# Optimization experiments

Measured on AMD Instinct MI355X. Metric: run time of the kernel, lower is better.

The kernel has to match this reference:

```python
import jax, jax.numpy as jnp
import numpy as np

B, S, H, NH, HD, P, MAXP = 2, 2048, 2048, 16, 128, 2048, 4096
EPS = 1e-06


def setup_inputs() -> dict:
    key = jax.random.key(0)
    ks = jax.random.split(key, 8)
    sc = lambda fan: 1.0 / np.sqrt(fan)
    hidden_states = jax.random.normal(ks[0], (B, S, H), jnp.float32)
    # rotary table: freqs[p] = p * inv_freq, duplicated (non-interleaved) -> [MAXP,1,1,HD]
    inv_freq = 1.0 / (500000.0 ** (np.arange(0, HD, 2, dtype=np.float32) / HD))
    ang = np.outer(np.arange(MAXP, dtype=np.float32), inv_freq)  # [MAXP, HD/2]
    freqs = jnp.asarray(np.concatenate([ang, ang], axis=-1).reshape(MAXP, 1, 1, HD), jnp.float32)
    positions = jnp.tile(jnp.arange(S, dtype=jnp.int32), B)  # [T] = [B*S]
    Wqk = jax.random.normal(ks[1], (2 * P, H), jnp.float32) * sc(H)
    Wv = jax.random.normal(ks[2], (P, H), jnp.float32) * sc(H)
    Wo = jax.random.normal(ks[3], (H, P), jnp.float32) * sc(P)
    conv1_w = jax.random.normal(ks[4], (H // 2, H, 2, 1), jnp.float32) * sc(2 * H)
    conv1_b = jax.random.normal(ks[5], (H // 2,), jnp.float32) * 0.01
    conv2_w = jax.random.normal(ks[6], (H, H // 2, 2, 1), jnp.float32) * sc(H)
    conv2_b = jax.random.normal(ks[7], (H,), jnp.float32) * 0.01
    ln_w = jnp.ones((H,), jnp.float32)
    lf1_cache = jnp.zeros((B, H, 1, 1), jnp.float32)
    lf2_cache = jnp.zeros((B, H // 2, 1, 1), jnp.float32)
    return dict(hidden_states=hidden_states, freqs=freqs, positions=positions,
                Wqk=Wqk, Wv=Wv, Wo=Wo, conv1_w=conv1_w, conv1_b=conv1_b,
                conv2_w=conv2_w, conv2_b=conv2_b, ln_w=ln_w,
                lf1_cache=lf1_cache, lf2_cache=lf2_cache)


def _rmsnorm(x, w, eps=EPS):
    return x * w * jax.lax.rsqrt(jnp.mean(x * x, axis=-1, keepdims=True) + eps)


def _rotate_half(x):
    x1, x2 = jnp.split(x, 2, axis=-1)
    return jnp.concatenate([-x2, x1], axis=-1)


def _forward(hidden_states, freqs, positions, Wqk, Wv, Wo,
             conv1_w, conv1_b, conv2_w, conv2_b, ln_w, lf1_cache, lf2_cache):
    # v projection on raw hidden states
    v = jnp.einsum('bsh,ph->bsp', hidden_states, Wv)  # [B,S,P]

    # --- LocalizedFiltering (causal (2,1) convs with 1-step caches) ---
    x = hidden_states                                     # [B,S,H]
    xc = jnp.concatenate([lf1_cache[:, :, 0, 0][:, None, :], x], axis=1)  # [B,S+1,H]
    w1a, w1b = conv1_w[:, :, 0, 0], conv1_w[:, :, 1, 0]   # [H/2,H]
    y1 = (jnp.einsum('bsh,oh->bso', xc[:, :-1], w1a)
          + jnp.einsum('bsh,oh->bso', xc[:, 1:], w1b) + conv1_b)  # [B,S,H/2]
    y1c = jnp.concatenate([lf2_cache[:, :, 0, 0][:, None, :], y1], axis=1)  # [B,S+1,H/2]
    w2a, w2b = conv2_w[:, :, 0, 0], conv2_w[:, :, 1, 0]   # [H,H/2]
    y2 = (jnp.einsum('bso,ho->bsh', y1c[:, :-1], w2a)
          + jnp.einsum('bso,ho->bsh', y1c[:, 1:], w2b) + conv2_b)  # [B,S,H]
    lf_out = _rmsnorm(y2 + x, ln_w)                       # [B,S,H]
    lf1_new = xc[:, -1][:, :, None, None]                 # [B,H,1,1]
    lf2_new = y1c[:, -1][:, :, None, None]                # [B,H/2,1,1]

    # --- QK projection + RoPE ---
    qk = jnp.einsum('bsh,ph->bsp', lf_out, Wqk).reshape(B, S, NH, 2 * HD)
    q, k = jnp.split(qk, 2, axis=-1)                      # [B,S,NH,HD] each
    f = freqs[positions].reshape(B, S, 1, HD)             # per-token angles
    cos_, sin_ = jnp.cos(f), jnp.sin(f)
    q = q * cos_ + _rotate_half(q) * sin_
    k = k * cos_ + _rotate_half(k) * sin_

    # --- causal SDPA ---
    scale = HD ** -0.5
    vh = v.reshape(B, S, NH, HD)
    scores = jnp.einsum('bqhd,bkhd->bhqk', q, k) * scale  # [B,NH,S,S]
    mask = jnp.tril(jnp.ones((S, S), bool))
    scores = jnp.where(mask, scores, jnp.float32(-1e30))
    probs = jax.nn.softmax(scores, axis=-1)
    attn = jnp.einsum('bhqk,bkhd->bqhd', probs, vh).reshape(B * S, P)

    output = attn @ Wo.T                                  # [T,H]
    return output, lf1_new, lf2_new


def reference(hidden_states, freqs, positions, Wqk, Wv, Wo,
              conv1_w, conv1_b, conv2_w, conv2_b, ln_w, lf1_cache, lf2_cache):
    return _forward(hidden_states, freqs, positions, Wqk, Wv, Wo,
                    conv1_w, conv1_b, conv2_w, conv2_b, ln_w, lf1_cache, lf2_cache)
```

## Files before the change

kernel.cpp:

```cpp
#include <hip/hip_runtime.h>
#include <hip/hip_bf16.h>
#include <stdint.h>

#define Bb 2
#define Ss 2048
#define Hh 2048
#define NHh 16
#define HDd 128
#define Pp 2048
#define Mm 4096

typedef __bf16 bf16x8 __attribute__((ext_vector_type(8)));
typedef float f32x4 __attribute__((ext_vector_type(4)));
typedef float f32x16 __attribute__((ext_vector_type(16)));
typedef __hip_bfloat16 bf16_t;

static __device__ __forceinline__ bf16_t f2b(float f) { return __float2bfloat16(f); }
static __device__ __forceinline__ float b2f(bf16_t b) { return __bfloat162float(b); }


__global__ void k_f2b(const float* __restrict__ src, bf16_t* __restrict__ dst, int n) {
  int stride = gridDim.x * blockDim.x;
  for (int i = blockIdx.x * blockDim.x + threadIdx.x; i < n; i += stride)
    dst[i] = f2b(src[i]);
}

__global__ void k_pack_conv1(const float* __restrict__ w, bf16_t* __restrict__ dst) {
  int stride = gridDim.x * blockDim.x;
  for (int i = blockIdx.x * blockDim.x + threadIdx.x; i < 1024 * 4096; i += stride) {
    int o = i >> 12, hp = i & 4095;
    int t = hp >> 11, h = hp & 2047;
    dst[i] = f2b(w[((size_t)o * 2048 + h) * 2 + t]);
  }
}

__global__ void k_pack_conv2(const float* __restrict__ w, bf16_t* __restrict__ dst) {
  int stride = gridDim.x * blockDim.x;
  for (int i = blockIdx.x * blockDim.x + threadIdx.x; i < 2048 * 2048; i += stride) {
    int o = i >> 11, cp = i & 2047;
    int t = cp >> 10, c = cp & 1023;
    dst[i] = f2b(w[((size_t)o * 1024 + c) * 2 + t]);
  }
}

__global__ void k_pack_x(const float* __restrict__ x, const float* __restrict__ lf1,
                         bf16_t* __restrict__ xcat) {
  int stride = gridDim.x * blockDim.x;
  for (int i = blockIdx.x * blockDim.x + threadIdx.x; i < Mm * Hh; i += stride) {
    int m = i >> 11, h = i & 2047;
    int b = m >> 11, s = m & 2047;
    float xv = x[i];
    xcat[(size_t)m * 4096 + 2048 + h] = f2b(xv);
    float xs = (s == 0) ? lf1[b * 2048 + h] : x[i - 2048];
    xcat[(size_t)m * 4096 + h] = f2b(xs);
  }
}

__global__ void k_pack_y1cat(const float* __restrict__ y1, const float* __restrict__ lf2,
                             bf16_t* __restrict__ y1cat) {
  int stride = gridDim.x * blockDim.x;
  for (int i = blockIdx.x * blockDim.x + threadIdx.x; i < Mm * 1024; i += stride) {
    int m = i >> 10, c = i & 1023;
    int b = m >> 11, s = m & 2047;
    y1cat[(size_t)m * 2048 + 1024 + c] = f2b(y1[i]);
    float ys = (s == 0) ? lf2[b * 1024 + c] : y1[i - 1024];
    y1cat[(size_t)m * 2048 + c] = f2b(ys);
  }
}

__global__ __launch_bounds__(256) void k_rmsnorm(const float* __restrict__ y2,
                                                 const float* __restrict__ x,
                                                 const float* __restrict__ w,
                                                 bf16_t* __restrict__ out) {
  int m = blockIdx.x;
  const float* yr = y2 + (size_t)m * 2048;
  const float* xr = x + (size_t)m * 2048;
  int tid = threadIdx.x;
  float t[8];
  float ss = 0.0f;
#pragma unroll
  for (int j = 0; j < 8; ++j) {
    int idx = tid + j * 256;
    float v = yr[idx] + xr[idx];
    t[j] = v;
    ss += v * v;
  }
#pragma unroll
  for (int o = 32; o >= 1; o >>= 1) ss += __shfl_xor(ss, o, 64);
  __shared__ float red[4];
  if ((tid & 63) == 0) red[tid >> 6] = ss;
  __syncthreads();
  float tot = red[0] + red[1] + red[2] + red[3];
  float rs = rsqrtf(tot * (1.0f / 2048.0f) + 1e-6f);
#pragma unroll
  for (int j = 0; j < 8; ++j) {
    int idx = tid + j * 256;
    out[(size_t)m * 2048 + idx] = f2b(t[j] * w[idx] * rs);
  }
}

__global__ __launch_bounds__(256) void k_rope(const bf16_t* __restrict__ qk,
                                              const float* __restrict__ freqs,
                                              const int* __restrict__ positions,
                                              bf16_t* __restrict__ qa, bf16_t* __restrict__ ka) {
  int m = blockIdx.x;
  int b = m >> 11, s = m & 2047;
  int pos = positions[m];
  const float* fr = freqs + (size_t)pos * HDd;
  const bf16_t* row = qk + (size_t)m * 4096;
  const float scale = 0.08838834764831845f;
#pragma unroll
  for (int it = 0; it < 8; ++it) {
    int p = it * 256 + threadIdx.x;
    int isk = p >> 10;
    int pp = p & 1023;
    int h = pp >> 6, d = pp & 63;
    float f = fr[d];
    float c = cosf(f), sn = sinf(f);
    float v0 = b2f(row[h * 256 + isk * 128 + d]);
    float v1 = b2f(row[h * 256 + isk * 128 + 64 + d]);
    float o0 = v0 * c - v1 * sn;
    float o1 = v1 * c + v0 * sn;
    float sc = isk ? 1.0f : scale;
    bf16_t* dst = (isk ? ka : qa) + ((size_t)(b * NHh + h) * Ss + s) * HDd;
    dst[d] = f2b(o0 * sc);
    dst[64 + d] = f2b(o1 * sc);
  }
}

__global__ __launch_bounds__(256) void k_vt(const bf16_t* __restrict__ v, bf16_t* __restrict__ vt) {
  int bh = blockIdx.x;
  int s0 = blockIdx.y * 64;
  int b = bh >> 4, h = bh & 15;
  __shared__ bf16_t tile[128][65];
#pragma unroll
  for (int it = 0; it < 32; ++it) {
    int idx = it * 256 + threadIdx.x;
    int sl = idx >> 7, d = idx & 127;
    tile[d][sl] = v[((size_t)(b * 2048 + s0 + sl)) * 2048 + h * 128 + d];
  }
  __syncthreads();
#pragma unroll
  for (int it = 0; it < 32; ++it) {
    int idx = it * 256 + threadIdx.x;
    int d = idx >> 6, sl = idx & 63;
    vt[((size_t)bh * 128 + d) * 2048 + s0 + sl] = tile[d][sl];
  }
}

__global__ void k_tails(const float* __restrict__ x, const float* __restrict__ y1,
                        float* __restrict__ out) {
  int i = blockIdx.x * 256 + threadIdx.x;
  if (i >= 4096 + 2048) return;
  const size_t off = (size_t)Mm * Hh;
  if (i < 4096) {
    int b = i >> 11, h = i & 2047;
    out[off + i] = x[((size_t)b * 2048 + 2047) * 2048 + h];
  } else {
    int j = i - 4096;
    int b = j >> 10, c = j & 1023;
    out[off + 4096 + j] = y1[((size_t)b * 2048 + 2047) * 1024 + c];
  }
}

template <int BF16_OUT, int HAS_BIAS>
__global__ __launch_bounds__(256) void gemm_bt_kernel(const bf16_t* __restrict__ A,
                                                      const bf16_t* __restrict__ Bw,
                                                      void* __restrict__ Cout,
                                                      const float* __restrict__ bias,
                                                      int M, int N, int K, int lda) {
  __shared__ bf16_t lA[128 * 64];
  __shared__ bf16_t lB[128 * 64];
  const int tid = threadIdx.x;
  const int lane = tid & 63;
  const int row0 = blockIdx.x * 128;
  const int col0 = blockIdx.y * 128;
  const int wr = ((tid >> 6) >> 1) * 64;
  const int wc = ((tid >> 6) & 1) * 64;
  const int lr = lane & 15;
  const int lg = lane >> 4;

  f32x4 acc[4][4];
#pragma unroll
  for (int i = 0; i < 4; ++i)
#pragma unroll
    for (int j = 0; j < 4; ++j) acc[i][j] = f32x4{0.f, 0.f, 0.f, 0.f};

  for (int k0 = 0; k0 < K; k0 += 64) {
    __syncthreads();
#pragma unroll
    for (int is = 0; is < 4; ++is) {
      const int e = is * 2048 + tid * 8;
      const int r = e >> 6, c = e & 63;
      __builtin_amdgcn_global_load_lds(
          (const __attribute__((address_space(1))) void*)(A + (size_t)(row0 + r) * lda + (k0 + c)),
          (__attribute__((address_space(3))) void*)(&lA[e]), 16, 0, 0);
      __builtin_amdgcn_global_load_lds(
          (const __attribute__((address_space(1))) void*)(Bw + (size_t)(col0 + r) * K + (k0 + c)),
          (__attribute__((address_space(3))) void*)(&lB[e]), 16, 0, 0);
    }
    __syncthreads();
#pragma unroll
    for (int ks = 0; ks < 2; ++ks) {
      bf16x8 af[4], bfg[4];
#pragma unroll
      for (int mi = 0; mi < 4; ++mi)
        af[mi] = *reinterpret_cast<const bf16x8*>(&lA[(wr + mi * 16 + lr) * 64 + ks * 32 + lg * 8]);
#pragma unroll
      for (int ni = 0; ni < 4; ++ni)
        bfg[ni] = *reinterpret_cast<const bf16x8*>(&lB[(wc + ni * 16 + lr) * 64 + ks * 32 + lg * 8]);
#pragma unroll
      for (int mi = 0; mi < 4; ++mi)
#pragma unroll
        for (int ni = 0; ni < 4; ++ni)
          acc[mi][ni] = __builtin_amdgcn_mfma_f32_16x16x32_bf16(af[mi], bfg[ni], acc[mi][ni], 0, 0, 0);
    }
  }
#pragma unroll
  for (int mi = 0; mi < 4; ++mi) {
#pragma unroll
    for (int ni = 0; ni < 4; ++ni) {
      const int cc = col0 + wc + ni * 16 + lr;
      float bv = HAS_BIAS ? bias[cc] : 0.0f;
#pragma unroll
      for (int r = 0; r < 4; ++r) {
        const int rr = row0 + wr + mi * 16 + lg * 4 + r;
        float v = acc[mi][ni][r] + bv;
        if (BF16_OUT)
          ((bf16_t*)Cout)[(size_t)rr * N + cc] = f2b(v);
        else
          ((float*)Cout)[(size_t)rr * N + cc] = v;
      }
    }
  }
}

__global__ __launch_bounds__(256) void k_attn2(const bf16_t* __restrict__ qa,
                                               const bf16_t* __restrict__ ka,
                                               const bf16_t* __restrict__ vt,
                                               bf16_t* __restrict__ attn_out) {
  __shared__ bf16_t kbuf[64 * 128];
  __shared__ bf16_t vbuf[128 * 64];
  __shared__ bf16_t pbuf[4][32 * 64];

  const int tid = threadIdx.x;
  const int wave = tid >> 6, lane = tid & 63;
  const int l31 = lane & 31, hi = lane >> 5;
  const int bh = blockIdx.x;
  const int q0b = blockIdx.y * 128;
  const int q0w = q0b + wave * 32;
  const int b = bh >> 4, h = bh & 15;

  const bf16_t* Q = qa + (size_t)bh * Ss * HDd;
  const bf16_t* K = ka + (size_t)bh * Ss * HDd;
  const bf16_t* V = vt + (size_t)bh * HDd * Ss;
  char* pw = (char*)&pbuf[wave][0];

  bf16x8 qf[8];
#pragma unroll
  for (int dc = 0; dc < 8; ++dc)
    qf[dc] = *reinterpret_cast<const bf16x8*>(&Q[(size_t)(q0w + l31) * HDd + dc * 16 + hi * 8]);

  f32x16 o[4];
#pragma unroll
  for (int db = 0; db < 4; ++db)
#pragma unroll
    for (int i = 0; i < 16; ++i) o[db][i] = 0.f;
  float mrun = -3e38f, lrun = 0.f;
  const int qrow = q0w + l31;

  const int nkt = q0b / 64 + 2;
  for (int kt = 0; kt < nkt; ++kt) {
    const int k0 = kt * 64;
    __syncthreads();
#pragma unroll
    for (int i = 0; i < 4; ++i) {
      const int kr = tid >> 2, ku = (tid & 3) + 4 * i;
      bf16x8 tk = *reinterpret_cast<const bf16x8*>(&K[(size_t)(k0 + kr) * HDd + ku * 8]);
      *reinterpret_cast<bf16x8*>((char*)kbuf + kr * 256 + ((ku * 16) ^ ((kr & 7) << 4))) = tk;
      const int vr = tid >> 1, vu = (tid & 1) * 4 + i;
      bf16x8 tv = *reinterpret_cast<const bf16x8*>(&V[(size_t)vr * Ss + k0 + vu * 8]);
      *reinterpret_cast<bf16x8*>((char*)vbuf + vr * 128 + ((vu * 16) ^ ((vr & 7) << 4))) = tv;
    }
    __syncthreads();
    if (k0 > q0w + 31) continue;

    f32x16 s0, s1;
#pragma unroll
    for (int i = 0; i < 16; ++i) { s0[i] = 0.f; s1[i] = 0.f; }
#pragma unroll
    for (int dc = 0; dc < 8; ++dc) {
      const int off = (dc * 32 + hi * 16) ^ ((l31 & 7) << 4);
      bf16x8 kf0 = *reinterpret_cast<const bf16x8*>((const char*)kbuf + l31 * 256 + off);
      bf16x8 kf1 = *reinterpret_cast<const bf16x8*>((const char*)kbuf + (32 + l31) * 256 + off);
      s0 = __builtin_amdgcn_mfma_f32_32x32x16_bf16(kf0, qf[dc], s0, 0, 0, 0);
      s1 = __builtin_amdgcn_mfma_f32_32x32x16_bf16(kf1, qf[dc], s1, 0, 0, 0);
    }
    if (k0 + 63 > q0w) {
#pragma unroll
      for (int reg = 0; reg < 16; ++reg) {
        const int key = k0 + (reg & 3) + 8 * (reg >> 2) + 4 * hi;
        if (key > qrow) s0[reg] = -1e30f;
        if (key + 32 > qrow) s1[reg] = -1e30f;
      }
    }
    float pm = fmaxf(s0[0], s1[0]);
#pragma unroll
    for (int reg = 1; reg < 16; ++reg) pm = fmaxf(pm, fmaxf(s0[reg], s1[reg]));
    pm = fmaxf(pm, __shfl_xor(pm, 32, 64));
    if (!__all(pm - mrun <= 8.0f)) {
      const float mnew = fmaxf(mrun, pm);
      const float alpha = __expf(mrun - mnew);
      lrun *= alpha;
#pragma unroll
      for (int reg = 0; reg < 16; ++reg) {
        const int r = (reg & 3) + 8 * (reg >> 2) + 4 * hi;
        const float ar = __shfl(alpha, r, 64);
        o[0][reg] *= ar; o[1][reg] *= ar; o[2][reg] *= ar; o[3][reg] *= ar;
      }
      mrun = mnew;
    }
    float psum = 0.f;
#pragma unroll
    for (int reg = 0; reg < 16; ++reg) {
      s0[reg] = __expf(s0[reg] - mrun); psum += s0[reg];
      s1[reg] = __expf(s1[reg] - mrun); psum += s1[reg];
    }
    psum += __shfl_xor(psum, 32, 64);
    lrun += psum;
#pragma unroll
    for (int g = 0; g < 4; ++g) {
      uint32_t w0, w1, w2, w3;
      asm("v_cvt_pk_bf16_f32 %0, %1, %2" : "=v"(w0) : "v"(s0[4 * g]), "v"(s0[4 * g + 1]));
      asm("v_cvt_pk_bf16_f32 %0, %1, %2" : "=v"(w1) : "v"(s0[4 * g + 2]), "v"(s0[4 * g + 3]));
      asm("v_cvt_pk_bf16_f32 %0, %1, %2" : "=v"(w2) : "v"(s1[4 * g]), "v"(s1[4 * g + 1]));
      asm("v_cvt_pk_bf16_f32 %0, %1, %2" : "=v"(w3) : "v"(s1[4 * g + 2]), "v"(s1[4 * g + 3]));
      const int key0 = 8 * g + 4 * hi;
      const int sw = (l31 & 7) << 4;
      *reinterpret_cast<uint2*>(pw + l31 * 128 + ((key0 * 2) ^ sw)) = uint2{w0, w1};
      *reinterpret_cast<uint2*>(pw + l31 * 128 + (((key0 + 32) * 2) ^ sw)) = uint2{w2, w3};
    }
#pragma unroll
    for (int kc = 0; kc < 4; ++kc) {
      bf16x8 pa = *reinterpret_cast<const bf16x8*>(
          pw + l31 * 128 + ((kc * 32 + hi * 16) ^ ((l31 & 7) << 4)));
#pragma unroll
      for (int db = 0; db < 4; ++db) {
        const int d = db * 32 + l31;
        bf16x8 vf = *reinterpret_cast<const bf16x8*>(
            (const char*)vbuf + d * 128 + ((kc * 32 + hi * 16) ^ ((d & 7) << 4)));
        o[db] = __builtin_amdgcn_mfma_f32_32x32x16_bf16(pa, vf, o[db], 0, 0, 0);
      }
    }
  }
  const float linv = 1.0f / lrun;
#pragma unroll
  for (int reg = 0; reg < 16; ++reg) {
    const int r = (reg & 3) + 8 * (reg >> 2) + 4 * hi;
    const float li = __shfl(linv, r, 64);
    const int qr = q0w + r;
#pragma unroll
    for (int db = 0; db < 4; ++db) {
      attn_out[(size_t)(b * 2048 + qr) * 2048 + h * 128 + db * 32 + l31] = f2b(o[db][reg] * li);
    }
  }
}

extern "C" void kernel_launch(void* const* d_in, const int* in_sizes, int n_in,
                              void* d_out, int out_size, void* d_ws, size_t ws_size,
                              hipStream_t stream) {
  const float* x     = (const float*)d_in[0];
  const float* freqs = (const float*)d_in[1];
  const int*   pos   = (const int*)d_in[2];
  const float* Wqk   = (const float*)d_in[3];
  const float* Wv    = (const float*)d_in[4];
  const float* Wo    = (const float*)d_in[5];
  const float* c1w   = (const float*)d_in[6];
  const float* c1b   = (const float*)d_in[7];
  const float* c2w   = (const float*)d_in[8];
  const float* c2b   = (const float*)d_in[9];
  const float* lnw   = (const float*)d_in[10];
  const float* lf1   = (const float*)d_in[11];
  const float* lf2   = (const float*)d_in[12];
  float* out = (float*)d_out;

  char* ws = (char*)d_ws;
  const size_t MB = 1024 * 1024;
  bf16_t* wv_bf  = (bf16_t*)(ws + 0 * MB);
  bf16_t* wqk_bf = (bf16_t*)(ws + 8 * MB);
  bf16_t* wo_bf  = (bf16_t*)(ws + 24 * MB);
  bf16_t* w1cat  = (bf16_t*)(ws + 32 * MB);
  bf16_t* w2cat  = (bf16_t*)(ws + 40 * MB);
  bf16_t* xcat   = (bf16_t*)(ws + 48 * MB);
  bf16_t* v_bf   = (bf16_t*)(ws + 80 * MB);
  float*  y1_f   = (float*)(ws + 96 * MB);
  bf16_t* y1cat  = (bf16_t*)(ws + 112 * MB);
  float*  y2_f   = (float*)(ws + 48 * MB);
  bf16_t* lfo_bf = (bf16_t*)(ws + 96 * MB);
  bf16_t* qk_bf  = (bf16_t*)(ws + 48 * MB);
  bf16_t* vt_att = (bf16_t*)(ws + 112 * MB);
  bf16_t* q_att  = (bf16_t*)(ws + 80 * MB);
  bf16_t* k_att  = (bf16_t*)(ws + 8 * MB);
  bf16_t* attn_b = (bf16_t*)(ws + 48 * MB);

  k_f2b<<<2048, 256, 0, stream>>>(Wv, wv_bf, 2048 * 2048);
  k_f2b<<<2048, 256, 0, stream>>>(Wqk, wqk_bf, 4096 * 2048);
  k_f2b<<<2048, 256, 0, stream>>>(Wo, wo_bf, 2048 * 2048);
  k_pack_conv1<<<2048, 256, 0, stream>>>(c1w, w1cat);
  k_pack_conv2<<<2048, 256, 0, stream>>>(c2w, w2cat);
  k_pack_x<<<2048, 256, 0, stream>>>(x, lf1, xcat);

  gemm_bt_kernel<1, 0><<<dim3(Mm / 128, 2048 / 128), 256, 0, stream>>>(
      xcat + 2048, wv_bf, v_bf, nullptr, Mm, 2048, 2048, 4096);
  gemm_bt_kernel<0, 1><<<dim3(Mm / 128, 1024 / 128), 256, 0, stream>>>(
      xcat, w1cat, y1_f, c1b, Mm, 1024, 4096, 4096);
  k_tails<<<24, 256, 0, stream>>>(x, y1_f, out);
  k_pack_y1cat<<<2048, 256, 0, stream>>>(y1_f, lf2, y1cat);
  gemm_bt_kernel<0, 1><<<dim3(Mm / 128, 2048 / 128), 256, 0, stream>>>(
      y1cat, w2cat, y2_f, c2b, Mm, 2048, 2048, 2048);
  k_rmsnorm<<<Mm, 256, 0, stream>>>(y2_f, x, lnw, lfo_bf);
  gemm_bt_kernel<1, 0><<<dim3(Mm / 128, 4096 / 128), 256, 0, stream>>>(
      lfo_bf, wqk_bf, qk_bf, nullptr, Mm, 4096, 2048, 2048);
  k_vt<<<dim3(Bb * NHh, Ss / 64), 256, 0, stream>>>(v_bf, vt_att);
  k_rope<<<Mm, 256, 0, stream>>>(qk_bf, freqs, pos, q_att, k_att);
  k_attn2<<<dim3(Bb * NHh, Ss / 128), 256, 0, stream>>>(q_att, k_att, vt_att, attn_b);
  gemm_bt_kernel<0, 0><<<dim3(Mm / 128, 2048 / 128), 256, 0, stream>>>(
      attn_b, wo_bf, out, nullptr, Mm, 2048, 2048, 2048);
}
```

Baseline: 680.9 us.

## Fuse RoPE, V transpose and y1cat packing into GEMM epilogues; pipeline attention loads

Adds epilogue variants to the GEMM template so the QK GEMM applies RoPE and writes head-major q/k directly, the V GEMM writes the transposed V layout, and the conv1 GEMM writes the shifted bf16 concat buffer itself. This removes the separate rope, transpose and pack kernels along with their intermediate round-trips through global memory. The attention kernel now issues the next K/V tile's global loads early into registers, raises wave priority around the MFMA blocks, and launches the longest causal query blocks first for load balance. It also reshuffles workspace offsets. The new epilogues add LDS staging and a sync, and y1 now flows through bf16 instead of fp32, which affects precision.

New measurement: 642.7 us. -5.6%, faster.

```diff
diff --git a/kernel.cpp b/kernel.cpp
--- a/kernel.cpp
+++ b/kernel.cpp
@@ -56,16 +56,11 @@
   }
 }
 
-__global__ void k_pack_y1cat(const float* __restrict__ y1, const float* __restrict__ lf2,
-                             bf16_t* __restrict__ y1cat) {
-  int stride = gridDim.x * blockDim.x;
-  for (int i = blockIdx.x * blockDim.x + threadIdx.x; i < Mm * 1024; i += stride) {
-    int m = i >> 10, c = i & 1023;
-    int b = m >> 11, s = m & 2047;
-    y1cat[(size_t)m * 2048 + 1024 + c] = f2b(y1[i]);
-    float ys = (s == 0) ? lf2[b * 1024 + c] : y1[i - 1024];
-    y1cat[(size_t)m * 2048 + c] = f2b(ys);
-  }
+__global__ void k_lf2fill(const float* __restrict__ lf2, bf16_t* __restrict__ y1cat) {
+  int i = blockIdx.x * 256 + threadIdx.x;
+  if (i >= 2048) return;
+  int b = i >> 10, c = i & 1023;
+  y1cat[(size_t)(b * 2048) * 2048 + c] = f2b(lf2[b * 1024 + c]);
 }
 
 __global__ __launch_bounds__(256) void k_rmsnorm(const float* __restrict__ y2,
@@ -99,56 +94,7 @@
   }
 }
 
-__global__ __launch_bounds__(256) void k_rope(const bf16_t* __restrict__ qk,
-                                              const float* __restrict__ freqs,
-                                              const int* __restrict__ positions,
-                                              bf16_t* __restrict__ qa, bf16_t* __restrict__ ka) {
-  int m = blockIdx.x;
-  int b = m >> 11, s = m & 2047;
-  int pos = positions[m];
-  const float* fr = freqs + (size_t)pos * HDd;
-  const bf16_t* row = qk + (size_t)m * 4096;
-  const float scale = 0.08838834764831845f;
-#pragma unroll
-  for (int it = 0; it < 8; ++it) {
-    int p = it * 256 + threadIdx.x;
-    int isk = p >> 10;
-    int pp = p & 1023;
-    int h = pp >> 6, d = pp & 63;
-    float f = fr[d];
-    float c = cosf(f), sn = sinf(f);
-    float v0 = b2f(row[h * 256 + isk * 128 + d]);
-    float v1 = b2f(row[h * 256 + isk * 128 + 64 + d]);
-    float o0 = v0 * c - v1 * sn;
-    float o1 = v1 * c + v0 * sn;
-    float sc = isk ? 1.0f : scale;
-    bf16_t* dst = (isk ? ka : qa) + ((size_t)(b * NHh + h) * Ss + s) * HDd;
-    dst[d] = f2b(o0 * sc);
-    dst[64 + d] = f2b(o1 * sc);
-  }
-}
-
-__global__ __launch_bounds__(256) void k_vt(const bf16_t* __restrict__ v, bf16_t* __restrict__ vt) {
-  int bh = blockIdx.x;
-  int s0 = blockIdx.y * 64;
-  int b = bh >> 4, h = bh & 15;
-  __shared__ bf16_t tile[128][65];
-#pragma unroll
-  for (int it = 0; it < 32; ++it) {
-    int idx = it * 256 + threadIdx.x;
-    int sl = idx >> 7, d = idx & 127;
-    tile[d][sl] = v[((size_t)(b * 2048 + s0 + sl)) * 2048 + h * 128 + d];
-  }
-  __syncthreads();
-#pragma unroll
-  for (int it = 0; it < 32; ++it) {
-    int idx = it * 256 + threadIdx.x;
-    int d = idx >> 6, sl = idx & 63;
-    vt[((size_t)bh * 128 + d) * 2048 + s0 + sl] = tile[d][sl];
-  }
-}
-
-__global__ void k_tails(const float* __restrict__ x, const float* __restrict__ y1,
+__global__ void k_tails(const float* __restrict__ x, const bf16_t* __restrict__ y1cat,
                         float* __restrict__ out) {
   int i = blockIdx.x * 256 + threadIdx.x;
   if (i >= 4096 + 2048) return;
@@ -159,16 +105,23 @@
   } else {
     int j = i - 4096;
     int b = j >> 10, c = j & 1023;
-    out[off + 4096 + j] = y1[((size_t)b * 2048 + 2047) * 1024 + c];
-  }
-}
-
-template <int BF16_OUT, int HAS_BIAS>
-__global__ __launch_bounds__(256) void gemm_bt_kernel(const bf16_t* __restrict__ A,
-                                                      const bf16_t* __restrict__ Bw,
-                                                      void* __restrict__ Cout,
-                                                      const float* __restrict__ bias,
-                                                      int M, int N, int K, int lda) {
+    out[off + 4096 + j] = b2f(y1cat[((size_t)b * 2048 + 2047) * 2048 + 1024 + c]);
+  }
+}
+
+#define EPI_F32 0
+#define EPI_Y1CAT 1
+#define EPI_ROPE 2
+#define EPI_VT 3
+
+template <int EPI, int HAS_BIAS>
+__global__ __launch_bounds__(256) void gemm_epi(const bf16_t* __restrict__ A,
+                                                const bf16_t* __restrict__ Bw,
+                                                void* __restrict__ C1, void* __restrict__ C2,
+                                                const float* __restrict__ bias,
+                                                const int* __restrict__ posp,
+                                                const float* __restrict__ freqs,
+                                                int M, int N, int K, int lda) {
   __shared__ bf16_t lA[128 * 64];
   __shared__ bf16_t lB[128 * 64];
   const int tid = threadIdx.x;
@@ -216,26 +169,99 @@
           acc[mi][ni] = __builtin_amdgcn_mfma_f32_16x16x32_bf16(af[mi], bfg[ni], acc[mi][ni], 0, 0, 0);
     }
   }
-#pragma unroll
-  for (int mi = 0; mi < 4; ++mi) {
-#pragma unroll
-    for (int ni = 0; ni < 4; ++ni) {
-      const int cc = col0 + wc + ni * 16 + lr;
-      float bv = HAS_BIAS ? bias[cc] : 0.0f;
-#pragma unroll
-      for (int r = 0; r < 4; ++r) {
-        const int rr = row0 + wr + mi * 16 + lg * 4 + r;
-        float v = acc[mi][ni][r] + bv;
-        if (BF16_OUT)
-          ((bf16_t*)Cout)[(size_t)rr * N + cc] = f2b(v);
-        else
-          ((float*)Cout)[(size_t)rr * N + cc] = v;
-      }
-    }
-  }
-}
-
-__global__ __launch_bounds__(256) void k_attn2(const bf16_t* __restrict__ qa,
+
+  if constexpr (EPI == EPI_F32) {
+#pragma unroll
+    for (int mi = 0; mi < 4; ++mi)
+#pragma unroll
+      for (int ni = 0; ni < 4; ++ni) {
+        const int cc = col0 + wc + ni * 16 + lr;
+        float bv = HAS_BIAS ? bias[cc] : 0.0f;
+#pragma unroll
+        for (int r = 0; r < 4; ++r) {
+          const int rr = row0 + wr + mi * 16 + lg * 4 + r;
+          ((float*)C1)[(size_t)rr * N + cc] = acc[mi][ni][r] + bv;
+        }
+      }
+  } else if constexpr (EPI == EPI_Y1CAT) {
+    bf16_t* y1cat = (bf16_t*)C1;
+#pragma unroll
+    for (int mi = 0; mi < 4; ++mi)
+#pragma unroll
+      for (int ni = 0; ni < 4; ++ni) {
+        const int cc = col0 + wc + ni * 16 + lr;
+        float bv = HAS_BIAS ? bias[cc] : 0.0f;
+#pragma unroll
+        for (int r = 0; r < 4; ++r) {
+          const int rr = row0 + wr + mi * 16 + lg * 4 + r;
+          bf16_t v = f2b(acc[mi][ni][r] + bv);
+          y1cat[(size_t)rr * 2048 + 1024 + cc] = v;
+          if ((rr & 2047) != 2047) y1cat[(size_t)(rr + 1) * 2048 + cc] = v;
+        }
+      }
+  } else if constexpr (EPI == EPI_ROPE) {
+    __shared__ bf16_t tile[128][136];
+#pragma unroll
+    for (int mi = 0; mi < 4; ++mi)
+#pragma unroll
+      for (int ni = 0; ni < 4; ++ni) {
+        const int cl = wc + ni * 16 + lr;
+#pragma unroll
+        for (int r = 0; r < 4; ++r) {
+          const int rl = wr + mi * 16 + lg * 4 + r;
+          tile[rl][cl] = f2b(acc[mi][ni][r]);
+        }
+      }
+    __syncthreads();
+    const int r = tid >> 1, half = tid & 1;
+    const int m = row0 + r;
+    const int s = m & 2047, bb = m >> 11;
+    const int cb = col0 >> 7, h = cb >> 1, isk = cb & 1;
+    const int pos = posp[m];
+    const float* fr = freqs + (size_t)pos * HDd;
+    const float qs = isk ? 1.0f : 0.08838834764831845f;
+    bf16_t* dst = (bf16_t*)(isk ? C2 : C1) + ((size_t)(bb * NHh + h) * Ss + s) * HDd + half * 64;
+#pragma unroll
+    for (int j = 0; j < 8; ++j) {
+      bf16x8 lo = *reinterpret_cast<const bf16x8*>(&tile[r][j * 8]);
+      bf16x8 hv = *reinterpret_cast<const bf16x8*>(&tile[r][64 + j * 8]);
+      bf16x8 ov;
+#pragma unroll
+      for (int e = 0; e < 8; ++e) {
+        float f = fr[j * 8 + e];
+        float sn, cs;
+        __sincosf(f, &sn, &cs);
+        float v0 = b2f((bf16_t)lo[e]), v1 = b2f((bf16_t)hv[e]);
+        float o = half ? (v1 * cs + v0 * sn) : (v0 * cs - v1 * sn);
+        ov[e] = (__bf16)f2b(o * qs);
+      }
+      *reinterpret_cast<bf16x8*>(dst + j * 8) = ov;
+    }
+  } else if constexpr (EPI == EPI_VT) {
+    __shared__ bf16_t ttile[128][136];
+#pragma unroll
+    for (int mi = 0; mi < 4; ++mi)
+#pragma unroll
+      for (int ni = 0; ni < 4; ++ni) {
+        const int cl = wc + ni * 16 + lr;
+#pragma unroll
+        for (int r = 0; r < 4; ++r) {
+          const int rl = wr + mi * 16 + lg * 4 + r;
+          ttile[cl][rl] = f2b(acc[mi][ni][r]);
+        }
+      }
+    __syncthreads();
+    const int d = tid >> 1, sc = tid & 1;
+    const int bb = row0 >> 11, s0 = row0 & 2047, h = col0 >> 7;
+    bf16_t* dst = (bf16_t*)C1 + ((size_t)(bb * NHh + h) * HDd + d) * Ss + s0 + sc * 64;
+#pragma unroll
+    for (int j = 0; j < 8; ++j)
+      *reinterpret_cast<bf16x8*>(dst + j * 8) =
+          *reinterpret_cast<const bf16x8*>(&ttile[d][sc * 64 + j * 8]);
+  }
+}
+
+__global__ __launch_bounds__(256) void k_attn3(const bf16_t* __restrict__ qa,
                                                const bf16_t* __restrict__ ka,
                                                const bf16_t* __restrict__ vt,
                                                bf16_t* __restrict__ attn_out) {
@@ -247,7 +273,9 @@
   const int wave = tid >> 6, lane = tid & 63;
   const int l31 = lane & 31, hi = lane >> 5;
   const int bh = blockIdx.x;
-  const int q0b = blockIdx.y * 128;
+  const int yy = blockIdx.y;
+  const int jq = (yy < 8) ? (15 - yy) : (yy - 8);
+  const int q0b = jq * 128;
   const int q0w = q0b + wave * 32;
   const int b = bh >> 4, h = bh & 15;
 
@@ -270,24 +298,40 @@
   const int qrow = q0w + l31;
 
   const int nkt = q0b / 64 + 2;
+  bf16x8 pk[4], pv[4];
+  auto loadt = [&](int kt) {
+    const int k0l = kt * 64;
+#pragma unroll
+    for (int i = 0; i < 4; ++i) {
+      pk[i] = *reinterpret_cast<const bf16x8*>(
+          &K[(size_t)(k0l + (tid >> 2)) * HDd + ((tid & 3) + 4 * i) * 8]);
+      pv[i] = *reinterpret_cast<const bf16x8*>(
+          &V[(size_t)(tid >> 1) * Ss + k0l + ((tid & 1) * 4 + i) * 8]);
+    }
+  };
+  loadt(0);
+
   for (int kt = 0; kt < nkt; ++kt) {
     const int k0 = kt * 64;
     __syncthreads();
-#pragma unroll
-    for (int i = 0; i < 4; ++i) {
-      const int kr = tid >> 2, ku = (tid & 3) + 4 * i;
-      bf16x8 tk = *reinterpret_cast<const bf16x8*>(&K[(size_t)(k0 + kr) * HDd + ku * 8]);
-      *reinterpret_cast<bf16x8*>((char*)kbuf + kr * 256 + ((ku * 16) ^ ((kr & 7) << 4))) = tk;
-      const int vr = tid >> 1, vu = (tid & 1) * 4 + i;
-      bf16x8 tv = *reinterpret_cast<const bf16x8*>(&V[(size_t)vr * Ss + k0 + vu * 8]);
-      *reinterpret_cast<bf16x8*>((char*)vbuf + vr * 128 + ((vu * 16) ^ ((vr & 7) << 4))) = tv;
-    }
-    __syncthreads();
+    {
+      const int kr = tid >> 2, vr = tid >> 1;
+#pragma unroll
+      for (int i = 0; i < 4; ++i) {
+        const int ku = (tid & 3) + 4 * i;
+        *reinterpret_cast<bf16x8*>((char*)kbuf + kr * 256 + ((ku * 16) ^ ((kr & 7) << 4))) = pk[i];
+        const int vu = (tid & 1) * 4 + i;
+        *reinterpret_cast<bf16x8*>((char*)vbuf + vr * 128 + ((vu * 16) ^ ((vr & 7) << 4))) = pv[i];
+      }
+    }
+    __syncthreads();
+    if (kt + 1 < nkt) loadt(kt + 1);
     if (k0 > q0w + 31) continue;
 
     f32x16 s0, s1;
 #pragma unroll
     for (int i = 0; i < 16; ++i) { s0[i] = 0.f; s1[i] = 0.f; }
+    __builtin_amdgcn_s_setprio(1);
 #pragma unroll
     for (int dc = 0; dc < 8; ++dc) {
       const int off = (dc * 32 + hi * 16) ^ ((l31 & 7) << 4);
@@ -296,6 +340,7 @@
       s0 = __builtin_amdgcn_mfma_f32_32x32x16_bf16(kf0, qf[dc], s0, 0, 0, 0);
       s1 = __builtin_amdgcn_mfma_f32_32x32x16_bf16(kf1, qf[dc], s1, 0, 0, 0);
     }
+    __builtin_amdgcn_s_setprio(0);
     if (k0 + 63 > q0w) {
 #pragma unroll
       for (int reg = 0; reg < 16; ++reg) {
@@ -340,6 +385,7 @@
       *reinterpret_cast<uint2*>(pw + l31 * 128 + ((key0 * 2) ^ sw)) = uint2{w0, w1};
       *reinterpret_cast<uint2*>(pw + l31 * 128 + (((key0 + 32) * 2) ^ sw)) = uint2{w2, w3};
     }
+    __builtin_amdgcn_s_setprio(1);
 #pragma unroll
     for (int kc = 0; kc < 4; ++kc) {
       bf16x8 pa = *reinterpret_cast<const bf16x8*>(
@@ -352,6 +398,7 @@
         o[db] = __builtin_amdgcn_mfma_f32_32x32x16_bf16(pa, vf, o[db], 0, 0, 0);
       }
     }
+    __builtin_amdgcn_s_setprio(0);
   }
   const float linv = 1.0f / lrun;
 #pragma unroll
@@ -387,20 +434,17 @@
   char* ws = (char*)d_ws;
   const size_t MB = 1024 * 1024;
   bf16_t* wv_bf  = (bf16_t*)(ws + 0 * MB);
-  bf16_t* wqk_bf = (bf16_t*)(ws + 8 * MB);
-  bf16_t* wo_bf  = (bf16_t*)(ws + 24 * MB);
-  bf16_t* w1cat  = (bf16_t*)(ws + 32 * MB);
+  bf16_t* w1cat  = (bf16_t*)(ws + 8 * MB);
+  bf16_t* wqk_bf = (bf16_t*)(ws + 16 * MB);
+  bf16_t* wo_bf  = (bf16_t*)(ws + 32 * MB);
   bf16_t* w2cat  = (bf16_t*)(ws + 40 * MB);
   bf16_t* xcat   = (bf16_t*)(ws + 48 * MB);
-  bf16_t* v_bf   = (bf16_t*)(ws + 80 * MB);
-  float*  y1_f   = (float*)(ws + 96 * MB);
-  bf16_t* y1cat  = (bf16_t*)(ws + 112 * MB);
+  bf16_t* y1cat  = (bf16_t*)(ws + 80 * MB);
+  bf16_t* vt_att = (bf16_t*)(ws + 96 * MB);
+  bf16_t* q_att  = (bf16_t*)(ws + 112 * MB);
   float*  y2_f   = (float*)(ws + 48 * MB);
-  bf16_t* lfo_bf = (bf16_t*)(ws + 96 * MB);
-  bf16_t* qk_bf  = (bf16_t*)(ws + 48 * MB);
-  bf16_t* vt_att = (bf16_t*)(ws + 112 * MB);
-  bf16_t* q_att  = (bf16_t*)(ws + 80 * MB);
-  bf16_t* k_att  = (bf16_t*)(ws + 8 * MB);
+  bf16_t* lfo_bf = (bf16_t*)(ws + 80 * MB);
+  bf16_t* k_att  = (bf16_t*)(ws + 0 * MB);
   bf16_t* attn_b = (bf16_t*)(ws + 48 * MB);
 
   k_f2b<<<2048, 256, 0, stream>>>(Wv, wv_bf, 2048 * 2048);
@@ -409,21 +453,19 @@
   k_pack_conv1<<<2048, 256, 0, stream>>>(c1w, w1cat);
   k_pack_conv2<<<2048, 256, 0, stream>>>(c2w, w2cat);
   k_pack_x<<<2048, 256, 0, stream>>>(x, lf1, xcat);
-
-  gemm_bt_kernel<1, 0><<<dim3(Mm / 128, 2048 / 128), 256, 0, stream>>>(
-      xcat + 2048, wv_bf, v_bf, nullptr, Mm, 2048, 2048, 4096);
-  gemm_bt_kernel<0, 1><<<dim3(Mm / 128, 1024 / 128), 256, 0, stream>>>(
-      xcat, w1cat, y1_f, c1b, Mm, 1024, 4096, 4096);
-  k_tails<<<24, 256, 0, stream>>>(x, y1_f, out);
-  k_pack_y1cat<<<2048, 256, 0, stream>>>(y1_f, lf2, y1cat);
-  gemm_bt_kernel<0, 1><<<dim3(Mm / 128, 2048 / 128), 256, 0, stream>>>(
-      y1cat, w2cat, y2_f, c2b, Mm, 2048, 2048, 2048);
+  k_lf2fill<<<8, 256, 0, stream>>>(lf2, y1cat);
+
+  gemm_epi<EPI_VT, 0><<<dim3(Mm / 128, 2048 / 128), 256, 0, stream>>>(
+      xcat + 2048, wv_bf, vt_att, nullptr, nullptr, nullptr, nullptr, Mm, 2048, 2048, 4096);
+  gemm_epi<EPI_Y1CAT, 1><<<dim3(Mm / 128, 1024 / 128), 256, 0, stream>>>(
+      xcat, w1cat, y1cat, nullptr, c1b, nullptr, nullptr, Mm, 1024, 4096, 4096);
+  k_tails<<<24, 256, 0, stream>>>(x, y1cat, out);
+  gemm_epi<EPI_F32, 1><<<dim3(Mm / 128, 2048 / 128), 256, 0, stream>>>(
+      y1cat, w2cat, y2_f, nullptr, c2b, nullptr, nullptr, Mm, 2048, 2048, 2048);
   k_rmsnorm<<<Mm, 256, 0, stream>>>(y2_f, x, lnw, lfo_bf);
-  gemm_bt_kernel<1, 0><<<dim3(Mm / 128, 4096 / 128), 256, 0, stream>>>(
-      lfo_bf, wqk_bf, qk_bf, nullptr, Mm, 4096, 2048, 2048);
-  k_vt<<<dim3(Bb * NHh, Ss / 64), 256, 0, stream>>>(v_bf, vt_att);
-  k_rope<<<Mm, 256, 0, stream>>>(qk_bf, freqs, pos, q_att, k_att);
-  k_attn2<<<dim3(Bb * NHh, Ss / 128), 256, 0, stream>>>(q_att, k_att, vt_att, attn_b);
-  gemm_bt_kernel<0, 0><<<dim3(Mm / 128, 2048 / 128), 256, 0, stream>>>(
-      attn_b, wo_bf, out, nullptr, Mm, 2048, 2048, 2048);
-}
+  gemm_epi<EPI_ROPE, 0><<<dim3(Mm / 128, 4096 / 128), 256, 0, stream>>>(
+      lfo_bf, wqk_bf, q_att, k_att, nullptr, pos, freqs, Mm, 4096, 2048, 2048);
+  k_attn3<<<dim3(Bb * NHh, Ss / 128), 256, 0, stream>>>(q_att, k_att, vt_att, attn_b);
+  gemm_epi<EPI_F32, 0><<<dim3(Mm / 128, 2048 / 128), 256, 0, stream>>>(
+      attn_b, wo_bf, out, nullptr, nullptr, nullptr, nullptr, Mm, 2048, 2048, 2048);
+}
```
